# Performance work log

Hardware: AMD Instinct MI355X
Metric: run time of the kernel (lower is better)

Reference implementation:

```python
import jax, jax.numpy as jnp
import numpy as np

# S6Layer dims: d_model=256; internal d_state=max(8,16//2)=8; expand=max(1.5,2*0.75)=1.5 -> d_inner=384
B, L, DM = 8, 4096, 256
DI, DS = 384, 8
CHUNK = 32  # seq_len > 64 path: chunked scan, state resets to 0 at every chunk (faithful to source)
EPS = 1e-5


def setup_inputs() -> dict:
    key = jax.random.key(0)
    ks = jax.random.split(key, 8)
    def w(k, shape, s=0.02):
        return jax.random.normal(k, shape, jnp.float32) * s
    return {
        "x": jax.random.normal(ks[0], (B, L, DM), jnp.float32),
        "gamma": jnp.ones((DM,), jnp.float32),
        "beta": jnp.zeros((DM,), jnp.float32),
        "W_in": w(ks[1], (3 * DI, DM)),
        "b_in": jnp.zeros((3 * DI,), jnp.float32),
        "W_dt": w(ks[2], (DI, DI)),
        "b_dt": jnp.zeros((DI,), jnp.float32),
        "A_log": jax.random.normal(ks[3], (DI, DS), jnp.float32),
        "D_vec": jax.random.normal(ks[4], (DI,), jnp.float32),
        "W_out": w(ks[5], (DM, DI)),
        "b_out": jnp.zeros((DM,), jnp.float32),
    }


def _layernorm(x, g, b):
    mu = jnp.mean(x, axis=-1, keepdims=True)
    var = jnp.mean(jnp.square(x - mu), axis=-1, keepdims=True)
    return (x - mu) * jax.lax.rsqrt(var + EPS) * g + b


def _chunked_scan(xp, dt, A):
    # xp, dt: [B, L, DI]; A: [DI, DS]. Each CHUNK-length block scans from h=0
    # (the torch code never propagates h across chunks for seq_len > 64).
    C = L // CHUNK
    xr = xp.reshape(B, C, CHUNK, DI)
    dtr = dt.reshape(B, C, CHUNK, DI)
    dA = jnp.exp(dtr[..., None] * A)              # [B, C, T, DI, DS]
    dA_t = jnp.moveaxis(dA, 2, 0)                 # [T, B, C, DI, DS]
    x_t = jnp.moveaxis(xr, 2, 0)                  # [T, B, C, DI]

    def step(h, inp):
        dA_i, x_i = inp
        h = h * dA_i + x_i[..., None]             # broadcast x over DS
        return h, jnp.sum(h, axis=-1)             # y_i: [B, C, DI]

    h0 = jnp.zeros((B, C, DI, DS), xp.dtype)
    _, ys = jax.lax.scan(step, h0, (dA_t, x_t))   # ys: [T, B, C, DI]
    return jnp.moveaxis(ys, 0, 2).reshape(B, L, DI)


def reference(x, gamma, beta, W_in, b_in, W_dt, b_dt, A_log, D_vec, W_out, b_out):
    residual = x
    xn = _layernorm(x, gamma, beta)
    xz = xn @ W_in.T + b_in                       # [B, L, 3*DI]
    x_proj, z, dt_in = jnp.split(xz, 3, axis=-1)
    x_proj = jax.nn.silu(x_proj)
    z = jax.nn.silu(z)
    dt = jax.nn.softplus(dt_in @ W_dt.T + b_dt)   # [B, L, DI]
    A = -jnp.exp(A_log)                           # [DI, DS]
    y = _chunked_scan(x_proj, dt, A)
    y = y * z + x_proj * D_vec
    return y @ W_out.T + b_out + residual
```

## Files before the change

### kernel.cpp

```cpp
#include <hip/hip_runtime.h>
#include <stdint.h>

#define B_  8
#define L_  4096
#define DM  256
#define DI  384
#define DS  8
#define M_  (B_*L_)

typedef float f32x4 __attribute__((ext_vector_type(4)));
typedef short s16x8 __attribute__((ext_vector_type(8)));

#define AS1(p) ((__attribute__((address_space(1))) void*)(p))
#define AS3(p) ((__attribute__((address_space(3))) void*)(p))

__device__ __forceinline__ unsigned short f2bf(float f) {
  union { float f; uint32_t u; } v; v.f = f;
  uint32_t r = v.u + 0x7FFFu + ((v.u >> 16) & 1u);
  return (unsigned short)(r >> 16);
}
__device__ __forceinline__ float bf2f(unsigned short h) {
  union { uint32_t u; float f; } v; v.u = ((uint32_t)h) << 16;
  return v.f;
}
__device__ __forceinline__ float silu_f(float x) {
  return x * __builtin_amdgcn_rcpf(1.f + __expf(-x));
}

__global__ __launch_bounds__(256) void cvt_kernel(
    const float* __restrict__ w0, const float* __restrict__ w2,
    const float* __restrict__ b_in,
    unsigned short* __restrict__ o0, unsigned short* __restrict__ o2,
    float* __restrict__ biasc) {
  int i = blockIdx.x * 256 + threadIdx.x;
  if (i < 3*DI*DM) o0[i] = f2bf(w0[i]);
  if (i < DM*DI)   o2[i] = f2bf(w2[i]);
  if (i < 2*DI)    biasc[i] = b_in[i];
}

__global__ __launch_bounds__(256) void prep_kernel(
    const float* __restrict__ W_in, const float* __restrict__ b_in,
    const float* __restrict__ W_dt, const float* __restrict__ b_dt,
    unsigned short* __restrict__ winb, float* __restrict__ biasc) {
  int nb = blockIdx.x;
  if (nb < DI) {
    int c = threadIdx.x;
    float acc = 0.f;
    for (int k = 0; k < DI; ++k)
      acc += W_dt[(size_t)nb*DI + k] * W_in[(size_t)(2*DI + k)*DM + c];
    winb[(size_t)(2*DI + nb)*DM + c] = f2bf(acc);
  } else {
    int n = (nb - DI)*256 + threadIdx.x;
    if (n < DI) {
      float acc = b_dt[n];
      for (int k = 0; k < DI; ++k)
        acc += W_dt[(size_t)n*DI + k] * b_in[2*DI + k];
      biasc[2*DI + n] = acc;
    }
  }
}

__global__ __launch_bounds__(256) void ln_kernel(
    const float* __restrict__ x, const float* __restrict__ gamma, const float* __restrict__ beta,
    unsigned short* __restrict__ xn) {
  int token = blockIdx.x * 4 + (threadIdx.x >> 6);
  int lane  = threadIdx.x & 63;
  const float4 v = *(const float4*)(x + (size_t)token*DM + lane*4);
  float s  = v.x + v.y + v.z + v.w;
  float ss = v.x*v.x + v.y*v.y + v.z*v.z + v.w*v.w;
  #pragma unroll
  for (int off = 32; off > 0; off >>= 1) {
    s  += __shfl_xor(s,  off, 64);
    ss += __shfl_xor(ss, off, 64);
  }
  float mean = s * (1.f/DM);
  float var  = ss * (1.f/DM) - mean*mean;
  float rstd = rsqrtf(var + 1e-5f);
  const float4 g = *(const float4*)(gamma + lane*4);
  const float4 b = *(const float4*)(beta  + lane*4);
  ushort4 o;
  o.x = f2bf((v.x - mean)*rstd*g.x + b.x);
  o.y = f2bf((v.y - mean)*rstd*g.y + b.y);
  o.z = f2bf((v.z - mean)*rstd*g.z + b.z);
  o.w = f2bf((v.w - mean)*rstd*g.w + b.w);
  *(ushort4*)(xn + (size_t)token*DM + lane*4) = o;
}

__global__ __launch_bounds__(256, 2) void s6_head(
    const unsigned short* __restrict__ xn,
    const unsigned short* __restrict__ Wb,
    const float* __restrict__ biasc,
    const float* __restrict__ A_log, const float* __restrict__ D_vec,
    unsigned short* __restrict__ yz)
{
  constexpr int K = 256, CPR = K/8;
  __shared__ unsigned short sB[64*K];
  __shared__ unsigned short sOut[3][128*64];
  const int t    = threadIdx.x;
  const int lane = t & 63;
  const int w    = t >> 6;
  const int fr   = lane & 15;
  const int fq   = lane >> 4;
  const int wm   = w * 32;

  const int q      = blockIdx.x;
  const int u      = q >> 3;
  const int mtile  = (q & 7) * 32 + (u & 31);
  const int panel  = u >> 5;
  const int mbase  = mtile * 128;
  const int chbase = panel * 64;

  const unsigned short* gA0 = xn + (size_t)(mbase + wm + fr)*K + fq*8;
  const unsigned short* gA1 = gA0 + (size_t)16*K;
  const unsigned short* sBrE = sB + (size_t)fr*K + ( fq      ^ (fr & 7))*8;
  const unsigned short* sBrO = sB + (size_t)fr*K + ((fq | 4) ^ (fr & 7))*8;

  #pragma unroll
  for (int sub = 0; sub < 3; ++sub) {
    const int nb = sub*DI + chbase;
    #pragma unroll
    for (int i = 0; i < (64*CPR)/256; ++i) {
      int c   = i*256 + t;
      int row = c / CPR;
      int j   = c - row*CPR;
      int jp  = (j & ~7) | ((j & 7) ^ (row & 7));
      __builtin_amdgcn_global_load_lds(AS1(Wb + (size_t)(nb + row)*K + jp*8),
                                       AS3(sB + c*8), 16, 0, 0);
    }
    __syncthreads();

    f32x4 acc[2][4];
    #pragma unroll
    for (int mi = 0; mi < 2; ++mi)
      #pragma unroll
      for (int ni = 0; ni < 4; ++ni) acc[mi][ni] = (f32x4){0.f, 0.f, 0.f, 0.f};

    #pragma unroll
    for (int kt = 0; kt < 8; ++kt) {
      s16x8 a0 = *(const s16x8*)(gA0 + kt*32);
      s16x8 a1 = *(const s16x8*)(gA1 + kt*32);
      const unsigned short* bb = (kt & 1) ? sBrO : sBrE;
      s16x8 bfr[4];
      #pragma unroll
      for (int ni = 0; ni < 4; ++ni)
        bfr[ni] = *(const s16x8*)(bb + ni*16*K + (kt >> 1)*64);
      #pragma unroll
      for (int ni = 0; ni < 4; ++ni) {
        acc[0][ni] = __builtin_amdgcn_mfma_f32_16x16x32_bf16(a0, bfr[ni], acc[0][ni], 0, 0, 0);
        acc[1][ni] = __builtin_amdgcn_mfma_f32_16x16x32_bf16(a1, bfr[ni], acc[1][ni], 0, 0, 0);
      }
    }

    #pragma unroll
    for (int ni = 0; ni < 4; ++ni) {
      float bv = biasc[nb + ni*16 + fr];
      int cn = (ni*16 + fr) ^ (fq << 4);
      #pragma unroll
      for (int mi = 0; mi < 2; ++mi) {
        int rm0 = wm + mi*16 + fq*4;
        #pragma unroll
        for (int r = 0; r < 4; ++r) {
          float c = acc[mi][ni][r] + bv;
          c = (sub < 2) ? silu_f(c)
                        : ((c > 20.f) ? c : __logf(1.f + __expf(c)));
          sOut[sub][(rm0 + r)*64 + cn] = f2bf(c);
        }
      }
    }
    __syncthreads();
  }

  {
    const int c  = t >> 6;
    const int d  = t & 63;
    const int ch = chbase + d;
    float a[DS], h[DS];
    #pragma unroll
    for (int s = 0; s < DS; ++s) { a[s] = -__expf(A_log[ch*DS + s]); h[s] = 0.f; }
    float Dv = D_vec[ch];
    unsigned short* yzp = yz + (size_t)(mbase + c*32)*DI + ch;
    for (int tt = 0; tt < 32; ++tt) {
      int idx = (c*32 + tt)*64 + (d ^ (((tt >> 2) & 3) << 4));
      float xv  = bf2f(sOut[0][idx]);
      float zv  = bf2f(sOut[1][idx]);
      float dtv = bf2f(sOut[2][idx]);
      float y = 0.f;
      #pragma unroll
      for (int s = 0; s < DS; ++s) {
        h[s] = h[s] * __expf(dtv * a[s]) + xv;
        y += h[s];
      }
      yzp[(size_t)tt*DI] = f2bf(y * zv + xv * Dv);
    }
  }
}

template<int KSTEPS, int MT>
__global__ __launch_bounds__(256, 3) void gemm_out(
    const unsigned short* __restrict__ A,
    const unsigned short* __restrict__ Bw,
    const float* __restrict__ bias,
    const float* __restrict__ resid, float* __restrict__ o_f)
{
  constexpr int K    = KSTEPS * 32;
  constexpr int CPR  = K / 8;
  __shared__ unsigned short sB[64*K];

  const int t    = threadIdx.x;
  const int lane = t & 63;
  const int w    = t >> 6;
  const int fr   = lane & 15;
  const int fq   = lane >> 4;
  const int wm   = w * 32;

  const int q    = blockIdx.y * 128 + blockIdx.x;
  const int bx2  = (q & 7) * 16 + ((q >> 3) & 15);
  const int by2  = q >> 7;
  const int mbase0 = bx2 * (128 * MT);
  const int nbase  = by2 * 64;

  #pragma unroll
  for (int i = 0; i < (64*CPR)/256; ++i) {
    int c   = i*256 + t;
    int row = c / CPR;
    int j   = c - row*CPR;
    int jp  = (j & ~7) | ((j & 7) ^ (row & 7));
    __builtin_amdgcn_global_load_lds(AS1(Bw + (size_t)(nbase + row)*K + jp*8),
                                     AS3(sB + c*8), 16, 0, 0);
  }

  const unsigned short* sBrE = sB + (size_t)fr*K + ( fq      ^ (fr & 7))*8;
  const unsigned short* sBrO = sB + (size_t)fr*K + ((fq | 4) ^ (fr & 7))*8;

  float bvv[4];
  #pragma unroll
  for (int ni = 0; ni < 4; ++ni) bvv[ni] = bias[nbase + ni*16 + fr];

  __syncthreads();

  #pragma unroll
  for (int mt = 0; mt < MT; ++mt) {
    const int mbase = mbase0 + mt*128;
    const unsigned short* gA0 = A + (size_t)(mbase + wm + fr)*K + fq*8;
    const unsigned short* gA1 = gA0 + (size_t)16*K;

    f32x4 acc[2][4];
    #pragma unroll
    for (int mi = 0; mi < 2; ++mi)
      #pragma unroll
      for (int ni = 0; ni < 4; ++ni) acc[mi][ni] = (f32x4){0.f, 0.f, 0.f, 0.f};

    #pragma unroll
    for (int kt = 0; kt < KSTEPS; ++kt) {
      s16x8 a0 = *(const s16x8*)(gA0 + kt*32);
      s16x8 a1 = *(const s16x8*)(gA1 + kt*32);
      const unsigned short* bb = (kt & 1) ? sBrO : sBrE;
      s16x8 bfr[4];
      #pragma unroll
      for (int ni = 0; ni < 4; ++ni)
        bfr[ni] = *(const s16x8*)(bb + ni*16*K + (kt >> 1)*64);
      #pragma unroll
      for (int ni = 0; ni < 4; ++ni) {
        acc[0][ni] = __builtin_amdgcn_mfma_f32_16x16x32_bf16(a0, bfr[ni], acc[0][ni], 0, 0, 0);
        acc[1][ni] = __builtin_amdgcn_mfma_f32_16x16x32_bf16(a1, bfr[ni], acc[1][ni], 0, 0, 0);
      }
    }

    #pragma unroll
    for (int ni = 0; ni < 4; ++ni) {
      int gn = nbase + ni*16 + fr;
      #pragma unroll
      for (int mi = 0; mi < 2; ++mi) {
        int gm0 = mbase + wm + mi*16 + fq*4;
        #pragma unroll
        for (int r = 0; r < 4; ++r) {
          size_t gm = (size_t)(gm0 + r);
          o_f[gm*DM + gn] = acc[mi][ni][r] + bvv[ni] + resid[gm*DM + gn];
        }
      }
    }
  }
}

extern "C" void kernel_launch(void* const* d_in, const int* in_sizes, int n_in,
                              void* d_out, int out_size, void* d_ws, size_t ws_size,
                              hipStream_t stream) {
  const float* x     = (const float*)d_in[0];
  const float* gamma = (const float*)d_in[1];
  const float* beta  = (const float*)d_in[2];
  const float* W_in  = (const float*)d_in[3];
  const float* b_in  = (const float*)d_in[4];
  const float* W_dt  = (const float*)d_in[5];
  const float* b_dt  = (const float*)d_in[6];
  const float* A_log = (const float*)d_in[7];
  const float* D_vec = (const float*)d_in[8];
  const float* W_out = (const float*)d_in[9];
  const float* b_out = (const float*)d_in[10];
  float* out = (float*)d_out;

  char* ws = (char*)d_ws;
  size_t off = 0;
  auto alloc = [&](size_t bytes) -> char* {
    char* p = ws + off; off += (bytes + 255) & ~(size_t)255; return p;
  };
  unsigned short* xn    = (unsigned short*)alloc((size_t)M_*DM*2);
  unsigned short* yzb   = (unsigned short*)alloc((size_t)M_*DI*2);
  unsigned short* winb  = (unsigned short*)alloc((size_t)3*DI*DM*2);
  unsigned short* woutb = (unsigned short*)alloc((size_t)DM*DI*2);
  float*          biasc = (float*)alloc((size_t)3*DI*4);

  cvt_kernel<<<dim3((3*DI*DM + 255)/256), 256, 0, stream>>>(W_in, W_out, b_in, winb, woutb, biasc);
  prep_kernel<<<dim3(DI + 2), 256, 0, stream>>>(W_in, b_in, W_dt, b_dt, winb, biasc);
  ln_kernel<<<dim3(M_/4), 256, 0, stream>>>(x, gamma, beta, xn);
  s6_head<<<dim3(6 * 256), 256, 0, stream>>>(xn, winb, biasc, A_log, D_vec, yzb);
  gemm_out<12, 2><<<dim3(128, DM/64), 256, 0, stream>>>(
      yzb, woutb, b_out, x, out);
}
```

Baseline: 218.7 us.

## Overlap weight staging with epilogue in s6_head and coalesce gemm_out stores

Measured after the change: 209.8 us. 1.04x faster.

```diff
diff --git a/kernel.cpp b/kernel.cpp
--- a/kernel.cpp
+++ b/kernel.cpp
@@ -115,8 +115,7 @@
   const unsigned short* sBrE = sB + (size_t)fr*K + ( fq      ^ (fr & 7))*8;
   const unsigned short* sBrO = sB + (size_t)fr*K + ((fq | 4) ^ (fr & 7))*8;
 
-  #pragma unroll
-  for (int sub = 0; sub < 3; ++sub) {
+  auto STAGE = [&](int sub) {
     const int nb = sub*DI + chbase;
     #pragma unroll
     for (int i = 0; i < (64*CPR)/256; ++i) {
@@ -127,14 +126,12 @@
       __builtin_amdgcn_global_load_lds(AS1(Wb + (size_t)(nb + row)*K + jp*8),
                                        AS3(sB + c*8), 16, 0, 0);
     }
-    __syncthreads();
-
-    f32x4 acc[2][4];
+  };
+  auto KLOOP = [&](f32x4 (&acc)[2][4]) {
     #pragma unroll
     for (int mi = 0; mi < 2; ++mi)
       #pragma unroll
       for (int ni = 0; ni < 4; ++ni) acc[mi][ni] = (f32x4){0.f, 0.f, 0.f, 0.f};
-
     #pragma unroll
     for (int kt = 0; kt < 8; ++kt) {
       s16x8 a0 = *(const s16x8*)(gA0 + kt*32);
@@ -150,7 +147,10 @@
         acc[1][ni] = __builtin_amdgcn_mfma_f32_16x16x32_bf16(a1, bfr[ni], acc[1][ni], 0, 0, 0);
       }
     }
-
+  };
+  auto EPI = [&](f32x4 (&acc)[2][4], int sub) {
+    const int nb = sub*DI + chbase;
+    const bool sl = (sub < 2);
     #pragma unroll
     for (int ni = 0; ni < 4; ++ni) {
       float bv = biasc[nb + ni*16 + fr];
@@ -161,14 +161,29 @@
         #pragma unroll
         for (int r = 0; r < 4; ++r) {
           float c = acc[mi][ni][r] + bv;
-          c = (sub < 2) ? silu_f(c)
-                        : ((c > 20.f) ? c : __logf(1.f + __expf(c)));
+          c = sl ? silu_f(c) : ((c > 20.f) ? c : __logf(1.f + __expf(c)));
           sOut[sub][(rm0 + r)*64 + cn] = f2bf(c);
         }
       }
     }
-    __syncthreads();
-  }
+  };
+
+  f32x4 aP[2][4], aC[2][4];
+  STAGE(0);
+  __syncthreads();
+  KLOOP(aP);
+  __syncthreads();
+  STAGE(1);
+  EPI(aP, 0);
+  __syncthreads();
+  KLOOP(aC);
+  __syncthreads();
+  STAGE(2);
+  EPI(aC, 1);
+  __syncthreads();
+  KLOOP(aP);
+  EPI(aP, 2);
+  __syncthreads();
 
   {
     const int c  = t >> 6;
@@ -195,16 +210,15 @@
   }
 }
 
-template<int KSTEPS, int MT>
 __global__ __launch_bounds__(256, 3) void gemm_out(
     const unsigned short* __restrict__ A,
     const unsigned short* __restrict__ Bw,
     const float* __restrict__ bias,
     const float* __restrict__ resid, float* __restrict__ o_f)
 {
-  constexpr int K    = KSTEPS * 32;
-  constexpr int CPR  = K / 8;
+  constexpr int K = 384, CPR = K/8;
   __shared__ unsigned short sB[64*K];
+  float* sC = (float*)sB;
 
   const int t    = threadIdx.x;
   const int lane = t & 63;
@@ -213,11 +227,11 @@
   const int fq   = lane >> 4;
   const int wm   = w * 32;
 
-  const int q    = blockIdx.y * 128 + blockIdx.x;
-  const int bx2  = (q & 7) * 16 + ((q >> 3) & 15);
-  const int by2  = q >> 7;
-  const int mbase0 = bx2 * (128 * MT);
-  const int nbase  = by2 * 64;
+  const int q    = blockIdx.y * 256 + blockIdx.x;
+  const int bx2  = (q & 7) * 32 + ((q >> 3) & 31);
+  const int by2  = q >> 8;
+  const int mbase = bx2 * 128;
+  const int nbase = by2 * 64;
 
   #pragma unroll
   for (int i = 0; i < (64*CPR)/256; ++i) {
@@ -238,47 +252,52 @@
 
   __syncthreads();
 
-  #pragma unroll
-  for (int mt = 0; mt < MT; ++mt) {
-    const int mbase = mbase0 + mt*128;
-    const unsigned short* gA0 = A + (size_t)(mbase + wm + fr)*K + fq*8;
-    const unsigned short* gA1 = gA0 + (size_t)16*K;
-
-    f32x4 acc[2][4];
+  const unsigned short* gA0 = A + (size_t)(mbase + wm + fr)*K + fq*8;
+  const unsigned short* gA1 = gA0 + (size_t)16*K;
+
+  f32x4 acc[2][4];
+  #pragma unroll
+  for (int mi = 0; mi < 2; ++mi)
+    #pragma unroll
+    for (int ni = 0; ni < 4; ++ni) acc[mi][ni] = (f32x4){0.f, 0.f, 0.f, 0.f};
+
+  #pragma unroll
+  for (int kt = 0; kt < 12; ++kt) {
+    s16x8 a0 = *(const s16x8*)(gA0 + kt*32);
+    s16x8 a1 = *(const s16x8*)(gA1 + kt*32);
+    const unsigned short* bb = (kt & 1) ? sBrO : sBrE;
+    s16x8 bfr[4];
+    #pragma unroll
+    for (int ni = 0; ni < 4; ++ni)
+      bfr[ni] = *(const s16x8*)(bb + ni*16*K + (kt >> 1)*64);
+    #pragma unroll
+    for (int ni = 0; ni < 4; ++ni) {
+      acc[0][ni] = __builtin_amdgcn_mfma_f32_16x16x32_bf16(a0, bfr[ni], acc[0][ni], 0, 0, 0);
+      acc[1][ni] = __builtin_amdgcn_mfma_f32_16x16x32_bf16(a1, bfr[ni], acc[1][ni], 0, 0, 0);
+    }
+  }
+
+  __syncthreads();
+
+  #pragma unroll
+  for (int ni = 0; ni < 4; ++ni)
     #pragma unroll
     for (int mi = 0; mi < 2; ++mi)
       #pragma unroll
-      for (int ni = 0; ni < 4; ++ni) acc[mi][ni] = (f32x4){0.f, 0.f, 0.f, 0.f};
-
-    #pragma unroll
-    for (int kt = 0; kt < KSTEPS; ++kt) {
-      s16x8 a0 = *(const s16x8*)(gA0 + kt*32);
-      s16x8 a1 = *(const s16x8*)(gA1 + kt*32);
-      const unsigned short* bb = (kt & 1) ? sBrO : sBrE;
-      s16x8 bfr[4];
-      #pragma unroll
-      for (int ni = 0; ni < 4; ++ni)
-        bfr[ni] = *(const s16x8*)(bb + ni*16*K + (kt >> 1)*64);
-      #pragma unroll
-      for (int ni = 0; ni < 4; ++ni) {
-        acc[0][ni] = __builtin_amdgcn_mfma_f32_16x16x32_bf16(a0, bfr[ni], acc[0][ni], 0, 0, 0);
-        acc[1][ni] = __builtin_amdgcn_mfma_f32_16x16x32_bf16(a1, bfr[ni], acc[1][ni], 0, 0, 0);
-      }
-    }
-
-    #pragma unroll
-    for (int ni = 0; ni < 4; ++ni) {
-      int gn = nbase + ni*16 + fr;
-      #pragma unroll
-      for (int mi = 0; mi < 2; ++mi) {
-        int gm0 = mbase + wm + mi*16 + fq*4;
-        #pragma unroll
-        for (int r = 0; r < 4; ++r) {
-          size_t gm = (size_t)(gm0 + r);
-          o_f[gm*DM + gn] = acc[mi][ni][r] + bvv[ni] + resid[gm*DM + gn];
-        }
-      }
-    }
+      for (int r = 0; r < 4; ++r)
+        sC[(wm + mi*16 + fq*4 + r)*72 + ni*16 + fr] = acc[mi][ni][r] + bvv[ni];
+
+  __syncthreads();
+
+  const int rr = t >> 4, cl = (t & 15) * 4;
+  #pragma unroll
+  for (int it = 0; it < 8; ++it) {
+    int row = rr + it*16;
+    const float4 c  = *(const float4*)&sC[row*72 + cl];
+    const float4 rv = *(const float4*)(resid + (size_t)(mbase + row)*DM + nbase + cl);
+    float4 o;
+    o.x = c.x + rv.x; o.y = c.y + rv.y; o.z = c.z + rv.z; o.w = c.w + rv.w;
+    *(float4*)(o_f + (size_t)(mbase + row)*DM + nbase + cl) = o;
   }
 }
 
@@ -313,6 +332,5 @@
   prep_kernel<<<dim3(DI + 2), 256, 0, stream>>>(W_in, b_in, W_dt, b_dt, winb, biasc);
   ln_kernel<<<dim3(M_/4), 256, 0, stream>>>(x, gamma, beta, xn);
   s6_head<<<dim3(6 * 256), 256, 0, stream>>>(xn, winb, biasc, A_log, D_vec, yzb);
-  gemm_out<12, 2><<<dim3(128, DM/64), 256, 0, stream>>>(
-      yzb, woutb, b_out, x, out);
-}
+  gemm_out<<<dim3(256, DM/64), 256, 0, stream>>>(yzb, woutb, b_out, x, out);
+}
```
